# Optimization experiments

Hardware: AMD Instinct MI355X
Metric: run time of the kernel (lower is better)

## Reference

```python
import jax, jax.numpy as jnp
import numpy as np

NUM_REQS = 8192
MAX_NUM_REQS = 16384
NUM_TOKENS = 16_777_216
MAX_CTX = 32768


def setup_inputs() -> dict:
    key = jax.random.key(0)
    k1, k2, k3 = jax.random.split(key, 3)
    # cumulative query start offsets: sorted, qsl[0]=0, qsl[-1]=NUM_TOKENS
    inner = jnp.sort(jax.random.randint(k1, (NUM_REQS - 1,), 0, NUM_TOKENS, dtype=jnp.int32))
    query_start_loc = jnp.concatenate([
        jnp.zeros((1,), jnp.int32), inner, jnp.full((1,), NUM_TOKENS, jnp.int32)
    ])
    idx_mapping = jax.random.randint(k2, (NUM_REQS,), 0, MAX_NUM_REQS, dtype=jnp.int32)
    num_computed_tokens = jax.random.randint(k3, (MAX_NUM_REQS,), 0, MAX_CTX, dtype=jnp.int32)
    pos = jnp.zeros((NUM_TOKENS,), jnp.int32)       # output buffer
    seq_lens = jnp.zeros((MAX_NUM_REQS,), jnp.int32)  # output buffer
    return {
        "idx_mapping": idx_mapping,
        "query_start_loc": query_start_loc,
        "num_computed_tokens": num_computed_tokens,
        "pos": pos,
        "seq_lens": seq_lens,
    }


def reference(idx_mapping, query_start_loc, num_computed_tokens, pos, seq_lens):
    num_reqs = idx_mapping.shape[0]            # static
    max_num_reqs = seq_lens.shape[0]           # static
    num_tokens = pos.shape[0]                  # static; == query_start_loc[-1] by construction

    # per-request query lengths and gathered computed-token counts
    query_lens = query_start_loc[1:] - query_start_loc[:-1]      # [num_reqs]
    nct = num_computed_tokens[idx_mapping]                       # [num_reqs]

    # seq_lens: [0:num_reqs] = nct + query_len, [num_reqs:] = 0
    seq_lens_out = jnp.zeros((max_num_reqs,), seq_lens.dtype).at[:num_reqs].set(
        (nct + query_lens).astype(seq_lens.dtype)
    )

    # pos: for each token t, find its owning request via searchsorted over
    # the ragged offsets, then pos[t] = nct[req] + (t - start[req]).
    t = jnp.arange(num_tokens, dtype=query_start_loc.dtype)      # [num_tokens]
    req = jnp.searchsorted(query_start_loc, t, side="right") - 1 # [num_tokens]
    req = jnp.clip(req, 0, num_reqs - 1)
    pos_out = (nct[req] + (t - query_start_loc[req])).astype(pos.dtype)

    return pos_out, seq_lens_out
```

## Files before the change

### kernel.cpp

```cpp
#include <hip/hip_runtime.h>


#define TPB 256
#define TILE_TOK 2048
#define SEQ_PER_BLOCK (TPB * 4)

__global__ __launch_bounds__(TPB) void prep_kernel(
    const int* __restrict__ idx_mapping,
    const int* __restrict__ qsl,
    const int* __restrict__ nct,
    int* __restrict__ tile_req,
    int* __restrict__ seq_out,
    int num_reqs, int max_num_reqs, int num_tokens,
    int num_tiles, int tile_blocks)
{
    int b = blockIdx.x;
    if (b < tile_blocks) {
        int tile = b * TPB + (int)threadIdx.x;
        if (tile >= num_tiles) return;
        long long tl = (long long)tile * TILE_TOK;
        int t = (tl >= num_tokens) ? (num_tokens - 1) : (int)tl;
        int l = 0, h = num_reqs + 1;
        while (h - l > 1) {
            int mid = (l + h) >> 1;
            if (qsl[mid] <= t) l = mid; else h = mid;
        }
        tile_req[tile] = l;
        return;
    }
    int i = (b - tile_blocks) * SEQ_PER_BLOCK + (int)threadIdx.x * 4;
    if (i >= max_num_reqs) return;
    if (i + 4 <= max_num_reqs) {
        int4 v;
        int* vp = (int*)&v;
        #pragma unroll
        for (int k = 0; k < 4; ++k) {
            int idx = i + k;
            int val = 0;
            if (idx < num_reqs)
                val = nct[idx_mapping[idx]] + (qsl[idx + 1] - qsl[idx]);
            vp[k] = val;
        }
        *(int4*)(seq_out + i) = v;
    } else {
        for (int idx = i; idx < max_num_reqs; ++idx) {
            int val = 0;
            if (idx < num_reqs)
                val = nct[idx_mapping[idx]] + (qsl[idx + 1] - qsl[idx]);
            seq_out[idx] = val;
        }
    }
}

__global__ __launch_bounds__(TPB) void pos_kernel(
    const int* __restrict__ idx_mapping,
    const int* __restrict__ qsl,
    const int* __restrict__ nct,
    const int* __restrict__ tile_req,
    int* __restrict__ pos_out,
    int num_reqs, int num_tokens)
{
    int tile = blockIdx.x;
    long long bsl = (long long)tile * TILE_TOK;
    int blockStart = (int)bsl;
    int tid = (int)threadIdx.x;

    int tfirst = blockStart + tid * 4;
    if (tfirst >= num_tokens) return;

    int r = tile_req[tile];
    int next = qsl[r + 1];
    int base = nct[idx_mapping[r]] - qsl[r];

    while (tfirst >= next) {
        ++r;
        next = qsl[r + 1];
        base = nct[idx_mapping[r]] - qsl[r];
    }

    #pragma unroll
    for (int g = 0; g < 2; ++g) {
        int tc = blockStart + g * (TPB * 4) + tid * 4;
        if (tc >= num_tokens) return;
        int4 v;
        int* vp = (int*)&v;
        int t = tc;
        #pragma unroll
        for (int k = 0; k < 4; ++k) {
            while (t >= next) {
                ++r;
                next = qsl[r + 1];
                base = nct[idx_mapping[r]] - qsl[r];
            }
            vp[k] = base + t;
            ++t;
        }
        if (tc + 4 <= num_tokens) {
            *(int4*)(pos_out + tc) = v;
        } else {
            for (int k = 0; k < num_tokens - tc; ++k) pos_out[tc + k] = vp[k];
        }
    }
}

extern "C" void kernel_launch(void* const* d_in, const int* in_sizes, int n_in,
                              void* d_out, int out_size, void* d_ws, size_t ws_size,
                              hipStream_t stream) {
    const int* idx_mapping = (const int*)d_in[0];
    const int* qsl         = (const int*)d_in[1];
    const int* nct         = (const int*)d_in[2];

    int num_reqs     = in_sizes[0];
    int max_num_reqs = in_sizes[2];
    int num_tokens   = in_sizes[3];

    int* out = (int*)d_out;
    int* pos_out = out;
    int* seq_out = out + num_tokens;
    int* tile_req = (int*)d_ws;

    int num_tiles   = (int)(((long long)num_tokens + TILE_TOK - 1) / TILE_TOK);
    int tile_blocks = (num_tiles + TPB - 1) / TPB;
    int seq_blocks  = (max_num_reqs + SEQ_PER_BLOCK - 1) / SEQ_PER_BLOCK;

    prep_kernel<<<dim3(tile_blocks + seq_blocks), dim3(TPB), 0, stream>>>(
        idx_mapping, qsl, nct, tile_req, seq_out,
        num_reqs, max_num_reqs, num_tokens, num_tiles, tile_blocks);

    pos_kernel<<<dim3(num_tiles), dim3(TPB), 0, stream>>>(
        idx_mapping, qsl, nct, tile_req, pos_out, num_reqs, num_tokens);
}
```

Before: 143.8 us.

## Precompute per-request base offsets and add tile-uniform fast path in pos kernel

The prep kernel now stores a per-request base (nct[idx_mapping[r]] - qsl[r]) and also computes the request boundary at the tile end, giving num_tiles+1 bounds. The pos kernel uses half-size tiles with one int4 per thread. It skips the per-token search when a tile lies inside a single request, and writes output with nontemporal stores. This removes the dependent gather chain from the hot loop and cuts search work for the common case. In exchange it adds an extra workspace array and a dependency on prep writing base_req before pos runs, and there are twice as many tiles.

```diff
diff --git a/kernel.cpp b/kernel.cpp
--- a/kernel.cpp
+++ b/kernel.cpp
@@ -2,104 +2,97 @@
 
 
 #define TPB 256
-#define TILE_TOK 2048
+#define TILE_TOK 1024
 #define SEQ_PER_BLOCK (TPB * 4)
+
+typedef int vint4 __attribute__((ext_vector_type(4)));
 
 __global__ __launch_bounds__(TPB) void prep_kernel(
     const int* __restrict__ idx_mapping,
     const int* __restrict__ qsl,
     const int* __restrict__ nct,
     int* __restrict__ tile_req,
+    int* __restrict__ base_req,
     int* __restrict__ seq_out,
     int num_reqs, int max_num_reqs, int num_tokens,
-    int num_tiles, int tile_blocks)
+    int bound_count, int bound_blocks)
 {
     int b = blockIdx.x;
-    if (b < tile_blocks) {
-        int tile = b * TPB + (int)threadIdx.x;
-        if (tile >= num_tiles) return;
-        long long tl = (long long)tile * TILE_TOK;
+    if (b < bound_blocks) {
+        int j = b * TPB + (int)threadIdx.x;
+        if (j >= bound_count) return;
+        long long tl = (long long)j * TILE_TOK;
         int t = (tl >= num_tokens) ? (num_tokens - 1) : (int)tl;
         int l = 0, h = num_reqs + 1;
         while (h - l > 1) {
             int mid = (l + h) >> 1;
             if (qsl[mid] <= t) l = mid; else h = mid;
         }
-        tile_req[tile] = l;
+        tile_req[j] = l;
         return;
     }
-    int i = (b - tile_blocks) * SEQ_PER_BLOCK + (int)threadIdx.x * 4;
+    int i = (b - bound_blocks) * SEQ_PER_BLOCK + (int)threadIdx.x * 4;
     if (i >= max_num_reqs) return;
+    vint4 v;
+    #pragma unroll
+    for (int k = 0; k < 4; ++k) {
+        int idx = i + k;
+        int val = 0;
+        if (idx < num_reqs) {
+            int q0 = qsl[idx], q1 = qsl[idx + 1];
+            int nb = nct[idx_mapping[idx]];
+            base_req[idx] = nb - q0;
+            val = nb + (q1 - q0);
+        }
+        v[k] = val;
+    }
     if (i + 4 <= max_num_reqs) {
-        int4 v;
-        int* vp = (int*)&v;
-        #pragma unroll
-        for (int k = 0; k < 4; ++k) {
-            int idx = i + k;
-            int val = 0;
-            if (idx < num_reqs)
-                val = nct[idx_mapping[idx]] + (qsl[idx + 1] - qsl[idx]);
-            vp[k] = val;
-        }
-        *(int4*)(seq_out + i) = v;
+        *(vint4*)(seq_out + i) = v;
     } else {
-        for (int idx = i; idx < max_num_reqs; ++idx) {
-            int val = 0;
-            if (idx < num_reqs)
-                val = nct[idx_mapping[idx]] + (qsl[idx + 1] - qsl[idx]);
-            seq_out[idx] = val;
-        }
+        for (int k = 0; k < max_num_reqs - i; ++k) seq_out[i + k] = v[k];
     }
 }
 
 __global__ __launch_bounds__(TPB) void pos_kernel(
-    const int* __restrict__ idx_mapping,
     const int* __restrict__ qsl,
-    const int* __restrict__ nct,
     const int* __restrict__ tile_req,
+    const int* __restrict__ base_req,
     int* __restrict__ pos_out,
-    int num_reqs, int num_tokens)
+    int num_tokens)
 {
     int tile = blockIdx.x;
-    long long bsl = (long long)tile * TILE_TOK;
-    int blockStart = (int)bsl;
-    int tid = (int)threadIdx.x;
+    int t = tile * TILE_TOK + (int)threadIdx.x * 4;
+    if (t >= num_tokens) return;
 
-    int tfirst = blockStart + tid * 4;
-    if (tfirst >= num_tokens) return;
+    int r0 = tile_req[tile];
+    int r1 = tile_req[tile + 1];
+    vint4 v;
 
-    int r = tile_req[tile];
-    int next = qsl[r + 1];
-    int base = nct[idx_mapping[r]] - qsl[r];
-
-    while (tfirst >= next) {
-        ++r;
-        next = qsl[r + 1];
-        base = nct[idx_mapping[r]] - qsl[r];
+    if (r0 == r1) {
+        int base = base_req[r0];
+        v[0] = t + base; v[1] = t + 1 + base;
+        v[2] = t + 2 + base; v[3] = t + 3 + base;
+    } else {
+        int r = r0;
+        while (qsl[r + 1] <= t) ++r;
+        int next = qsl[r + 1];
+        int base = base_req[r];
+        #pragma unroll
+        for (int k = 0; k < 4; ++k) {
+            int tk = t + k;
+            while (tk >= next) {
+                ++r;
+                next = qsl[r + 1];
+                base = base_req[r];
+            }
+            v[k] = base + tk;
+        }
     }
 
-    #pragma unroll
-    for (int g = 0; g < 2; ++g) {
-        int tc = blockStart + g * (TPB * 4) + tid * 4;
-        if (tc >= num_tokens) return;
-        int4 v;
-        int* vp = (int*)&v;
-        int t = tc;
-        #pragma unroll
-        for (int k = 0; k < 4; ++k) {
-            while (t >= next) {
-                ++r;
-                next = qsl[r + 1];
-                base = nct[idx_mapping[r]] - qsl[r];
-            }
-            vp[k] = base + t;
-            ++t;
-        }
-        if (tc + 4 <= num_tokens) {
-            *(int4*)(pos_out + tc) = v;
-        } else {
-            for (int k = 0; k < num_tokens - tc; ++k) pos_out[tc + k] = vp[k];
-        }
+    if (t + 4 <= num_tokens) {
+        __builtin_nontemporal_store(v, (vint4*)(pos_out + t));
+    } else {
+        for (int k = 0; k < num_tokens - t; ++k) pos_out[t + k] = v[k];
     }
 }
 
@@ -117,16 +110,19 @@
     int* out = (int*)d_out;
     int* pos_out = out;
     int* seq_out = out + num_tokens;
-    int* tile_req = (int*)d_ws;
 
     int num_tiles   = (int)(((long long)num_tokens + TILE_TOK - 1) / TILE_TOK);
-    int tile_blocks = (num_tiles + TPB - 1) / TPB;
-    int seq_blocks  = (max_num_reqs + SEQ_PER_BLOCK - 1) / SEQ_PER_BLOCK;
+    int bound_count = num_tiles + 1;
+    int* tile_req = (int*)d_ws;
+    int* base_req = tile_req + (bound_count + 3) / 4 * 4;
 
-    prep_kernel<<<dim3(tile_blocks + seq_blocks), dim3(TPB), 0, stream>>>(
-        idx_mapping, qsl, nct, tile_req, seq_out,
-        num_reqs, max_num_reqs, num_tokens, num_tiles, tile_blocks);
+    int bound_blocks = (bound_count + TPB - 1) / TPB;
+    int seq_blocks   = (max_num_reqs + SEQ_PER_BLOCK - 1) / SEQ_PER_BLOCK;
+
+    prep_kernel<<<dim3(bound_blocks + seq_blocks), dim3(TPB), 0, stream>>>(
+        idx_mapping, qsl, nct, tile_req, base_req, seq_out,
+        num_reqs, max_num_reqs, num_tokens, bound_count, bound_blocks);
 
     pos_kernel<<<dim3(num_tiles), dim3(TPB), 0, stream>>>(
-        idx_mapping, qsl, nct, tile_req, pos_out, num_reqs, num_tokens);
+        qsl, tile_req, base_req, pos_out, num_tokens);
 }
```

Measured after the change: 119.5 us (median of 2 runs). 16.9% less time.
